# Kernel tuning notes

Measured on AMD Instinct MI355X. Metric: run time of the kernel, lower is better.

## Reference

```python
import jax, jax.numpy as jnp
import numpy as np

N_NODES = 50000
N_EDGES = 1600000
IN_CH = 128
OUT_CH = 128


def setup_inputs() -> dict:
    key = jax.random.key(0)
    k1, k2, k3, k4, k5 = jax.random.split(key, 5)
    x = jax.random.normal(k1, (N_NODES, IN_CH), dtype=jnp.float32)
    # edge_index[0] = destination (row), edge_index[1] = source (col)
    edge_index = jax.random.randint(k2, (2, N_EDGES), 0, N_NODES, dtype=jnp.int64)
    # Linear parameters (PyTorch default init: U(-1/sqrt(fan_in), 1/sqrt(fan_in)))
    bound = 1.0 / np.sqrt(IN_CH)
    W = jax.random.uniform(k3, (OUT_CH, IN_CH), dtype=jnp.float32, minval=-bound, maxval=bound)
    b = jax.random.uniform(k4, (OUT_CH,), dtype=jnp.float32, minval=-bound, maxval=bound)
    return {"x": x, "edge_index": edge_index, "W": W, "b": b}


def reference(x, edge_index, W, b) -> jnp.ndarray:
    # Linear projection: h = x @ W^T + b  -> [N, OUT_CH]
    h = jnp.einsum("nd,od->no", x, W) + b
    # spmm sum aggregation: out[dst] = sum_{edges e: dst(e)=dst} h[src(e)]
    dst = edge_index[0]
    src = edge_index[1]
    out = jax.ops.segment_sum(h[src], dst, num_segments=N_NODES)
    return out
```

## Files before the change

### kernel.cpp

```cpp
#include <hip/hip_runtime.h>

constexpr int N  = 50000;
constexpr int E  = 1600000;
constexpr int CH = 128;

constexpr int BSZ  = 64;
constexpr int NB   = (N + BSZ - 1) / BSZ;
constexpr int CAP  = 2560;
constexpr int SRTCAP = CAP + BSZ * 31 + 64;
constexpr int PBLK = 256;
constexpr int EPB  = E / PBLK;
constexpr int GEMM_BLOCKS = N / 16;

constexpr size_t H_OFF     = 0;
constexpr size_t H_SZ      = (size_t)(N + 1) * CH * 2;
constexpr size_t PAIRS_OFF = H_OFF + H_SZ;
constexpr size_t PAIRS_SZ  = (size_t)NB * CAP * 4;
constexpr size_t GCUR_OFF  = PAIRS_OFF + PAIRS_SZ;
constexpr size_t GCUR_SZ   = 3328;
constexpr size_t REQUIRED  = GCUR_OFF + GCUR_SZ;
constexpr size_t FB_REQUIRED = H_SZ;

static __device__ __forceinline__ ushort f2bf(float f) {
    unsigned u = __float_as_uint(f);
    return (ushort)((u + 0x7fffu + ((u >> 16) & 1u)) >> 16);
}
static __device__ __forceinline__ float bf_lo(unsigned u) { return __uint_as_float(u << 16); }
static __device__ __forceinline__ float bf_hi(unsigned u) { return __uint_as_float(u & 0xffff0000u); }

typedef __attribute__((ext_vector_type(8))) short bf16x8;
typedef __attribute__((ext_vector_type(4))) float f32x4;

static __device__ __forceinline__ void gemm_body(int gb, int tid,
                                                 const float* __restrict__ x,
                                                 const float* __restrict__ W,
                                                 const float* __restrict__ bias,
                                                 ushort* __restrict__ h) {
    const int m    = tid & 15;
    const int q    = (tid >> 4) & 3;
    const int wave = tid >> 6;
    const int r0   = gb * 16;
    const int c0   = wave * 32;

    const float* xrow = x + (size_t)(r0 + m) * CH + q * 8;
    const float* wr0  = W + (size_t)(c0 + m) * CH + q * 8;
    const float* wr1  = wr0 + 16 * CH;

    f32x4 acc0 = {0.f, 0.f, 0.f, 0.f};
    f32x4 acc1 = {0.f, 0.f, 0.f, 0.f};

#pragma unroll
    for (int kc = 0; kc < CH; kc += 32) {
        float4 xa = *(const float4*)(xrow + kc);
        float4 xb = *(const float4*)(xrow + kc + 4);
        float4 wa0 = *(const float4*)(wr0 + kc);
        float4 wb0 = *(const float4*)(wr0 + kc + 4);
        float4 wa1 = *(const float4*)(wr1 + kc);
        float4 wb1 = *(const float4*)(wr1 + kc + 4);
        bf16x8 a, b0, b1;
        a[0] = (short)f2bf(xa.x); a[1] = (short)f2bf(xa.y);
        a[2] = (short)f2bf(xa.z); a[3] = (short)f2bf(xa.w);
        a[4] = (short)f2bf(xb.x); a[5] = (short)f2bf(xb.y);
        a[6] = (short)f2bf(xb.z); a[7] = (short)f2bf(xb.w);
        b0[0] = (short)f2bf(wa0.x); b0[1] = (short)f2bf(wa0.y);
        b0[2] = (short)f2bf(wa0.z); b0[3] = (short)f2bf(wa0.w);
        b0[4] = (short)f2bf(wb0.x); b0[5] = (short)f2bf(wb0.y);
        b0[6] = (short)f2bf(wb0.z); b0[7] = (short)f2bf(wb0.w);
        b1[0] = (short)f2bf(wa1.x); b1[1] = (short)f2bf(wa1.y);
        b1[2] = (short)f2bf(wa1.z); b1[3] = (short)f2bf(wa1.w);
        b1[4] = (short)f2bf(wb1.x); b1[5] = (short)f2bf(wb1.y);
        b1[6] = (short)f2bf(wb1.z); b1[7] = (short)f2bf(wb1.w);
        acc0 = __builtin_amdgcn_mfma_f32_16x16x32_bf16(a, b0, acc0, 0, 0, 0);
        acc1 = __builtin_amdgcn_mfma_f32_16x16x32_bf16(a, b1, acc1, 0, 0, 0);
    }

    const int col0 = c0 + m;
    const float bb0 = bias[col0];
    const float bb1 = bias[col0 + 16];
#pragma unroll
    for (int r = 0; r < 4; r++) {
        size_t row = (size_t)(r0 + q * 4 + r) * CH;
        h[row + col0]      = f2bf(acc0[r] + bb0);
        h[row + col0 + 16] = f2bf(acc1[r] + bb1);
    }
}

__global__ __launch_bounds__(256) void gemm_and_scatter(const float* __restrict__ x,
                                                        const float* __restrict__ W,
                                                        const float* __restrict__ bias,
                                                        ushort* __restrict__ h,
                                                        const int* __restrict__ ei,
                                                        int* __restrict__ gcur,
                                                        unsigned* __restrict__ pairs) {
    __shared__ unsigned raw[EPB];
    __shared__ ushort   srt16[EPB];
    __shared__ int cnt[NB];
    __shared__ int lstart[NB];
    __shared__ int gpos[NB];
    __shared__ int cur[NB];
    __shared__ int wsum[4];
    const int bid = blockIdx.x;
    const int tid = threadIdx.x;

    if (bid >= PBLK) {
        gemm_body(bid - PBLK, tid, x, W, bias, h);
        return;
    }

    const int k = bid;
    const int* dp = ei + k * EPB;
    const int* sp = ei + E + k * EPB;

    if (bid == 0 && tid < 64) ((unsigned*)(h + (size_t)N * CH))[tid] = 0u;

    for (int j = tid; j < NB; j += 256) cnt[j] = 0;
    __syncthreads();
    for (int i = tid; i < EPB; i += 256) {
        int d = dp[i], s = sp[i];
        unsigned w = ((unsigned)(d >> 6) << 22) | ((unsigned)(d & (BSZ - 1)) << 16) | (unsigned)s;
        raw[i] = w;
        atomicAdd(&cnt[w >> 22], 1);
    }
    __syncthreads();

    for (int j = tid; j < NB; j += 256) {
        int c = cnt[j];
        gpos[j] = j * CAP + (c ? atomicAdd(&gcur[j], c) : 0);
    }

    {
        const int base = tid * 4;
        int s = 0;
#pragma unroll
        for (int i = 0; i < 4; i++) { int j = base + i; if (j < NB) s += cnt[j]; }
        const int lane = tid & 63;
        const int wid  = tid >> 6;
        int incl = s;
#pragma unroll
        for (int o = 1; o < 64; o <<= 1) {
            int u = __shfl_up(incl, o);
            if (lane >= o) incl += u;
        }
        if (lane == 63) wsum[wid] = incl;
        __syncthreads();
        int run = incl - s;
        for (int w = 0; w < wid; w++) run += wsum[w];
#pragma unroll
        for (int i = 0; i < 4; i++) {
            int j = base + i;
            if (j < NB) { lstart[j] = run; cur[j] = run; run += cnt[j]; }
        }
    }
    __syncthreads();

    for (int i = tid; i < EPB; i += 256) {
        int p = atomicAdd(&cur[raw[i] >> 22], 1);
        srt16[p] = (ushort)i;
    }
    __syncthreads();

    for (int i = tid; i < EPB; i += 256) {
        unsigned w = raw[srt16[i]];
        int bkt = w >> 22;
        int gdst = gpos[bkt] + (i - lstart[bkt]);
        if (gdst < (bkt + 1) * CAP)
            pairs[gdst] = w;
    }
}

__global__ __launch_bounds__(512, 2) void agg_fused(const ushort* __restrict__ h,
                                                    const unsigned* __restrict__ pairs,
                                                    const int* __restrict__ gcur,
                                                    float* __restrict__ out) {
    __shared__ unsigned raw[CAP];
    __shared__ ushort   srt[SRTCAP];
    __shared__ int hist[BSZ], offs[BSZ], cur[BSZ], cpad[BSZ];
    const int b = blockIdx.x, t = threadIdx.x;
    const int cnt = min(gcur[b], CAP);
    const int wave = t >> 6;
    const int lane = t & 63;
    const int quarter = lane >> 4;
    const int cq      = lane & 15;

    if (t < BSZ) hist[t] = 0;
    __syncthreads();

    const unsigned* slab = pairs + (size_t)b * CAP;
    for (int i = t; i < cnt; i += 512) {
        unsigned w = slab[i];
        raw[i] = w;
        atomicAdd(&hist[(w >> 16) & (BSZ - 1)], 1);
    }
    __syncthreads();

    if (t < BSZ) {
        int c  = hist[t];
        int cp = (c + 31) & ~31;
        int incl = cp;
#pragma unroll
        for (int o = 1; o < 64; o <<= 1) {
            int u = __shfl_up(incl, o);
            if (lane >= o) incl += u;
        }
        offs[t] = incl - cp;
        cur[t]  = incl - cp;
        cpad[t] = cp;
    }
    __syncthreads();

    const int tot = offs[BSZ - 1] + cpad[BSZ - 1];
    for (int i = t; i < tot; i += 512) srt[i] = (ushort)N;
    __syncthreads();
    for (int i = t; i < cnt; i += 512) {
        unsigned w = raw[i];
        int p = atomicAdd(&cur[(w >> 16) & (BSZ - 1)], 1);
        srt[p] = (ushort)(w & 0xffffu);
    }
    __syncthreads();

    const ushort* hp = h + (size_t)cq * 8;

#pragma unroll 1
    for (int j = 0; j < 8; j++) {
        const int nl = wave * 8 + j;
        const int st = offs[nl];
        const int cp = cpad[nl];
        float a0 = 0.f, a1 = 0.f, a2 = 0.f, a3 = 0.f;
        float a4 = 0.f, a5 = 0.f, a6 = 0.f, a7 = 0.f;
        for (int i = 0; i < cp; i += 32) {
            const int e0 = st + i + quarter;
            int sidx[8];
#pragma unroll
            for (int u = 0; u < 8; u++) sidx[u] = srt[e0 + 4 * u];
            uint4 v[8];
#pragma unroll
            for (int u = 0; u < 8; u++) v[u] = *(const uint4*)(hp + (size_t)sidx[u] * CH);
#pragma unroll
            for (int u = 0; u < 8; u++) {
                a0 += bf_lo(v[u].x); a1 += bf_hi(v[u].x);
                a2 += bf_lo(v[u].y); a3 += bf_hi(v[u].y);
                a4 += bf_lo(v[u].z); a5 += bf_hi(v[u].z);
                a6 += bf_lo(v[u].w); a7 += bf_hi(v[u].w);
            }
        }
        a0 += __shfl_xor(a0, 16); a0 += __shfl_xor(a0, 32);
        a1 += __shfl_xor(a1, 16); a1 += __shfl_xor(a1, 32);
        a2 += __shfl_xor(a2, 16); a2 += __shfl_xor(a2, 32);
        a3 += __shfl_xor(a3, 16); a3 += __shfl_xor(a3, 32);
        a4 += __shfl_xor(a4, 16); a4 += __shfl_xor(a4, 32);
        a5 += __shfl_xor(a5, 16); a5 += __shfl_xor(a5, 32);
        a6 += __shfl_xor(a6, 16); a6 += __shfl_xor(a6, 32);
        a7 += __shfl_xor(a7, 16); a7 += __shfl_xor(a7, 32);
        const int n = b * BSZ + nl;
        if (quarter == 0 && n < N) {
            float* op = out + (size_t)n * CH + cq * 8;
            *(float4*)(op)     = make_float4(a0, a1, a2, a3);
            *(float4*)(op + 4) = make_float4(a4, a5, a6, a7);
        }
    }
}

__global__ __launch_bounds__(256) void gemm_only(const float* __restrict__ x,
                                                 const float* __restrict__ W,
                                                 const float* __restrict__ bias,
                                                 ushort* __restrict__ h) {
    gemm_body(blockIdx.x, threadIdx.x, x, W, bias, h);
}

__global__ void atomic_agg(const ushort* __restrict__ h, const int* __restrict__ ei,
                           float* __restrict__ out) {
    int tid = blockIdx.x * blockDim.x + threadIdx.x;
    int e  = tid >> 5;
    int cg = (tid & 31) * 4;
    if (e < E) {
        int d = ei[e];
        int s = ei[E + e];
        ushort4 v = *(const ushort4*)(h + (size_t)s * CH + cg);
        float* o = out + (size_t)d * CH + cg;
        atomicAdd(o + 0, __uint_as_float((unsigned)v.x << 16));
        atomicAdd(o + 1, __uint_as_float((unsigned)v.y << 16));
        atomicAdd(o + 2, __uint_as_float((unsigned)v.z << 16));
        atomicAdd(o + 3, __uint_as_float((unsigned)v.w << 16));
    }
}

extern "C" void kernel_launch(void* const* d_in, const int* in_sizes, int n_in,
                              void* d_out, int out_size, void* d_ws, size_t ws_size,
                              hipStream_t stream) {
    const float* x  = (const float*)d_in[0];
    const int*   ei = (const int*)d_in[1];
    const float* W  = (const float*)d_in[2];
    const float* b  = (const float*)d_in[3];
    float* out = (float*)d_out;

    char* ws = (char*)d_ws;
    ushort* h = (ushort*)(ws + H_OFF);

    if (ws_size >= REQUIRED) {
        unsigned* pairs = (unsigned*)(ws + PAIRS_OFF);
        int*      gcur  = (int*)(ws + GCUR_OFF);

        hipMemsetAsync(gcur, 0, NB * sizeof(int), stream);
        gemm_and_scatter<<<PBLK + GEMM_BLOCKS, 256, 0, stream>>>(x, W, b, h, ei, gcur, pairs);
        agg_fused<<<NB, 512, 0, stream>>>(h, pairs, gcur, out);
    } else if (ws_size >= FB_REQUIRED) {
        gemm_only<<<GEMM_BLOCKS, 256, 0, stream>>>(x, W, b, h);
        hipMemsetAsync(out, 0, (size_t)out_size * sizeof(float), stream);
        int total = E * 32;
        atomic_agg<<<(total + 255) / 256, 256, 0, stream>>>(h, ei, out);
    }
}
```

Before: 178.6 us.

## Software-pipeline gather loads across iterations in the aggregation loop

The per-node edge loop is restructured so each iteration issues the next half-batch of h-row gathers before accumulating the current one. Loads are double-buffered in registers (A/B halves) instead of issuing all 8 loads and then stalling on them. The sentinel fill of the sorted index buffer is extended by 32 entries so the lookahead never reads uninitialized slots. Launch bounds are relaxed to a waves-per-EU range, letting the compiler trade occupancy for registers; this risks lower occupancy.

```diff
diff --git a/kernel.cpp b/kernel.cpp
--- a/kernel.cpp
+++ b/kernel.cpp
@@ -168,10 +168,15 @@
     }
 }
 
-__global__ __launch_bounds__(512, 2) void agg_fused(const ushort* __restrict__ h,
-                                                    const unsigned* __restrict__ pairs,
-                                                    const int* __restrict__ gcur,
-                                                    float* __restrict__ out) {
+#define ACC8(v) do { \
+    a0 += bf_lo((v).x); a1 += bf_hi((v).x); a2 += bf_lo((v).y); a3 += bf_hi((v).y); \
+    a4 += bf_lo((v).z); a5 += bf_hi((v).z); a6 += bf_lo((v).w); a7 += bf_hi((v).w); } while (0)
+
+__global__ __launch_bounds__(512) __attribute__((amdgpu_waves_per_eu(2, 6)))
+void agg_fused(const ushort* __restrict__ h,
+               const unsigned* __restrict__ pairs,
+               const int* __restrict__ gcur,
+               float* __restrict__ out) {
     __shared__ unsigned raw[CAP];
     __shared__ ushort   srt[SRTCAP];
     __shared__ int hist[BSZ], offs[BSZ], cur[BSZ], cpad[BSZ];
@@ -209,7 +214,8 @@
     __syncthreads();
 
     const int tot = offs[BSZ - 1] + cpad[BSZ - 1];
-    for (int i = t; i < tot; i += 512) srt[i] = (ushort)N;
+    const int fill = min(tot + 32, SRTCAP);
+    for (int i = t; i < fill; i += 512) srt[i] = (ushort)N;
     __syncthreads();
     for (int i = t; i < cnt; i += 512) {
         unsigned w = raw[i];
@@ -227,21 +233,28 @@
         const int cp = cpad[nl];
         float a0 = 0.f, a1 = 0.f, a2 = 0.f, a3 = 0.f;
         float a4 = 0.f, a5 = 0.f, a6 = 0.f, a7 = 0.f;
+        int base = st + quarter;
+        int sA0 = srt[base], sA1 = srt[base + 4], sA2 = srt[base + 8], sA3 = srt[base + 12];
+        uint4 vA0 = *(const uint4*)(hp + (size_t)sA0 * CH);
+        uint4 vA1 = *(const uint4*)(hp + (size_t)sA1 * CH);
+        uint4 vA2 = *(const uint4*)(hp + (size_t)sA2 * CH);
+        uint4 vA3 = *(const uint4*)(hp + (size_t)sA3 * CH);
+#pragma unroll 1
         for (int i = 0; i < cp; i += 32) {
-            const int e0 = st + i + quarter;
-            int sidx[8];
-#pragma unroll
-            for (int u = 0; u < 8; u++) sidx[u] = srt[e0 + 4 * u];
-            uint4 v[8];
-#pragma unroll
-            for (int u = 0; u < 8; u++) v[u] = *(const uint4*)(hp + (size_t)sidx[u] * CH);
-#pragma unroll
-            for (int u = 0; u < 8; u++) {
-                a0 += bf_lo(v[u].x); a1 += bf_hi(v[u].x);
-                a2 += bf_lo(v[u].y); a3 += bf_hi(v[u].y);
-                a4 += bf_lo(v[u].z); a5 += bf_hi(v[u].z);
-                a6 += bf_lo(v[u].w); a7 += bf_hi(v[u].w);
-            }
+            int sB0 = srt[base + 16], sB1 = srt[base + 20], sB2 = srt[base + 24], sB3 = srt[base + 28];
+            uint4 vB0 = *(const uint4*)(hp + (size_t)sB0 * CH);
+            uint4 vB1 = *(const uint4*)(hp + (size_t)sB1 * CH);
+            uint4 vB2 = *(const uint4*)(hp + (size_t)sB2 * CH);
+            uint4 vB3 = *(const uint4*)(hp + (size_t)sB3 * CH);
+            ACC8(vA0); ACC8(vA1); ACC8(vA2); ACC8(vA3);
+            const int nb = base + ((i + 32 < cp) ? 32 : 0);
+            sA0 = srt[nb]; sA1 = srt[nb + 4]; sA2 = srt[nb + 8]; sA3 = srt[nb + 12];
+            vA0 = *(const uint4*)(hp + (size_t)sA0 * CH);
+            vA1 = *(const uint4*)(hp + (size_t)sA1 * CH);
+            vA2 = *(const uint4*)(hp + (size_t)sA2 * CH);
+            vA3 = *(const uint4*)(hp + (size_t)sA3 * CH);
+            ACC8(vB0); ACC8(vB1); ACC8(vB2); ACC8(vB3);
+            base += 32;
         }
         a0 += __shfl_xor(a0, 16); a0 += __shfl_xor(a0, 32);
         a1 += __shfl_xor(a1, 16); a1 += __shfl_xor(a1, 32);
```

Measured after the change: 175.5 us. No clear change (-1.7%).
